# Kernel optimization log

Measured on AMD Instinct MI355X. Metric: run time of the kernel, lower is better.

Reference implementation:

```python
import jax, jax.numpy as jnp
import numpy as np

B = 262144      # batch (many robot-timestep samples)
IN_LEN = 32     # input_len
S = 64          # internal_state_len
M = 32          # message_len
P = 4           # num_ports
H = 100         # hidden_layer_size
L = 50          # lstm_hidden_size
O = 16          # output_len


def _linear_init(key, out_f, in_f):
    # torch.nn.Linear default init: U(-1/sqrt(in_f), 1/sqrt(in_f)) for W and b
    kw, kb = jax.random.split(key)
    bound = 1.0 / np.sqrt(in_f)
    W = jax.random.uniform(kw, (out_f, in_f), jnp.float32, -bound, bound)
    b = jax.random.uniform(kb, (out_f,), jnp.float32, -bound, bound)
    return W, b


def setup_inputs() -> dict:
    key = jax.random.key(0)
    ks = jax.random.split(key, 20)
    obs = jax.random.normal(ks[0], (B, IN_LEN), jnp.float32)
    messages_in = jax.random.normal(ks[1], (P, B, M), jnp.float32)
    h_lstm = jax.random.normal(ks[2], (B, L), jnp.float32)
    c_lstm = jax.random.normal(ks[3], (B, L), jnp.float32)

    W_in, b_in = _linear_init(ks[4], S, IN_LEN)
    # per-port message MLPs, stacked on a leading port axis
    msg1 = [_linear_init(jax.random.fold_in(ks[5], p), H, S) for p in range(P)]
    msg2 = [_linear_init(jax.random.fold_in(ks[6], p), M, H) for p in range(P)]
    msg_W1 = jnp.stack([w for w, _ in msg1])  # [P, H, S]
    msg_b1 = jnp.stack([b for _, b in msg1])  # [P, H]
    msg_W2 = jnp.stack([w for w, _ in msg2])  # [P, M, H]
    msg_b2 = jnp.stack([b for _, b in msg2])  # [P, M]

    # LSTMCell(S + M*P -> L); torch gate order i, f, g, o; init U(-1/sqrt(L), 1/sqrt(L))
    bl = 1.0 / np.sqrt(L)
    W_ih = jax.random.uniform(ks[7], (4 * L, S + M * P), jnp.float32, -bl, bl)
    W_hh = jax.random.uniform(ks[8], (4 * L, L), jnp.float32, -bl, bl)
    b_ih = jax.random.uniform(ks[9], (4 * L,), jnp.float32, -bl, bl)
    b_hh = jax.random.uniform(ks[10], (4 * L,), jnp.float32, -bl, bl)

    W_u1, b_u1 = _linear_init(ks[11], H, L)
    W_u2, b_u2 = _linear_init(ks[12], H, H)
    W_u3, b_u3 = _linear_init(ks[13], S, H)
    W_mu, b_mu = _linear_init(ks[14], O, S)
    W_var, b_var = _linear_init(ks[15], O, S)
    max_logvar = jnp.ones((1, O), jnp.float32) / 2.0
    min_logvar = -jnp.ones((1, O), jnp.float32) * 10.0

    return dict(obs=obs, messages_in=messages_in, h_lstm=h_lstm, c_lstm=c_lstm,
                W_in=W_in, b_in=b_in, msg_W1=msg_W1, msg_b1=msg_b1,
                msg_W2=msg_W2, msg_b2=msg_b2, W_ih=W_ih, W_hh=W_hh,
                b_ih=b_ih, b_hh=b_hh, W_u1=W_u1, b_u1=b_u1, W_u2=W_u2,
                b_u2=b_u2, W_u3=W_u3, b_u3=b_u3, W_mu=W_mu, b_mu=b_mu,
                W_var=W_var, b_var=b_var, max_logvar=max_logvar,
                min_logvar=min_logvar)


def reference(obs, messages_in, h_lstm, c_lstm, W_in, b_in, msg_W1, msg_b1,
              msg_W2, msg_b2, W_ih, W_hh, b_ih, b_hh, W_u1, b_u1, W_u2, b_u2,
              W_u3, b_u3, W_mu, b_mu, W_var, b_var, max_logvar, min_logvar):
    # run_input_function
    x = jax.nn.relu(obs @ W_in.T + b_in)                       # [B, S]

    # compute_messages_out_function: batched over ports (all ports occupied)
    m1 = jax.nn.relu(jnp.einsum('bs,phs->pbh', x, msg_W1) + msg_b1[:, None, :])
    msgs_out = jnp.einsum('pbh,pmh->pbm', m1, msg_W2) + msg_b2[:, None, :]  # [P, B, M]

    # compute_aggregation_function: concat incoming messages along feature dim
    agg = jnp.transpose(messages_in, (1, 0, 2)).reshape(obs.shape[0], -1)  # [B, P*M]
    h_mbar = jnp.concatenate([x, agg], axis=-1)                # [B, S + P*M]

    # status_update_function: one LSTMCell step (torch gate order i, f, g, o)
    gates = h_mbar @ W_ih.T + b_ih + h_lstm @ W_hh.T + b_hh    # [B, 4L]
    i, f, g, o = jnp.split(gates, 4, axis=-1)
    c_new = jax.nn.sigmoid(f) * c_lstm + jax.nn.sigmoid(i) * jnp.tanh(g)
    h_new = jax.nn.sigmoid(o) * jnp.tanh(c_new)                # [B, L]
    h2 = jax.nn.relu(h_new @ W_u1.T + b_u1)
    h2 = jax.nn.relu(h2 @ W_u2.T + b_u2)
    h2 = h2 @ W_u3.T + b_u3                                    # new internal state [B, S]

    # compute_output_function with soft logvar clamping
    mu = h2 @ W_mu.T + b_mu                                    # [B, O]
    logvar = h2 @ W_var.T + b_var
    logvar = max_logvar - jax.nn.softplus(max_logvar - logvar)
    logvar = min_logvar + jax.nn.softplus(logvar - min_logvar)
    var = jnp.exp(logvar)

    msgs_flat = jnp.transpose(msgs_out, (1, 0, 2)).reshape(obs.shape[0], -1)  # [B, P*M]
    # concat all outputs: mu(16) var(16) msgs(128) h2(64) h_new(50) c_new(50) = 324
    return jnp.concatenate([mu, var, msgs_flat, h2, h_new, c_new], axis=-1)
```

## Files before the change

### kernel.cpp

```cpp
#include <hip/hip_runtime.h>

typedef __bf16 bf16_t;
typedef __bf16 bf16x8 __attribute__((ext_vector_type(8)));
typedef float f32x4 __attribute__((ext_vector_type(4)));

#define B_TOTAL 262144
#define OUTC 324
#define ROWS 64

#define OFF_WIN   0
#define OFF_WG    2048
#define OFF_WM1   67584
#define OFF_WM2   96256
#define OFF_WU1   112640
#define OFF_WU2   119808
#define OFF_WU3   134144
#define OFF_WMV2  142336
#define BF16_TOTAL 145920

__global__ void prep_kernel(const float* W_in, const float* msg_W1, const float* msg_W2,
                            const float* W_ih, const float* W_hh, const float* b_ih, const float* b_hh,
                            const float* W_u1, const float* W_u2, const float* W_u3, const float* b_u3f,
                            const float* W_mu, const float* W_var, const float* b_mu, const float* b_var,
                            bf16_t* wb, float* bg, float* bmv) {
  int tid = blockIdx.x * blockDim.x + threadIdx.x;
  int nth = gridDim.x * blockDim.x;
  for (int i = tid; i < 2048; i += nth) wb[OFF_WIN + i] = (bf16_t)W_in[i];
  for (int i = tid; i < 65536; i += nth) {
    int n = i >> 8, k = i & 255;
    int g = n >> 6, j = n & 63;
    float v = 0.f;
    if (j < 50) {
      int r = g * 50 + j;
      if (k < 192) v = W_ih[r * 192 + k];
      else if (k < 242) v = W_hh[r * 50 + (k - 192)];
    }
    wb[OFF_WG + i] = (bf16_t)v;
  }
  for (int i = tid; i < 256; i += nth) {
    int g = i >> 6, j = i & 63;
    bg[i] = (j < 50) ? (b_ih[g * 50 + j] + b_hh[g * 50 + j]) : 0.f;
  }
  for (int i = tid; i < 4 * 112 * 64; i += nth) {
    int p = i / (112 * 64); int rem = i % (112 * 64); int n = rem >> 6, k = rem & 63;
    wb[OFF_WM1 + i] = (bf16_t)((n < 100) ? msg_W1[(p * 100 + n) * 64 + k] : 0.f);
  }
  for (int i = tid; i < 4 * 32 * 128; i += nth) {
    int p = i / (32 * 128); int rem = i % (32 * 128); int n = rem >> 7, k = rem & 127;
    wb[OFF_WM2 + i] = (bf16_t)((k < 100) ? msg_W2[(p * 32 + n) * 100 + k] : 0.f);
  }
  for (int i = tid; i < 112 * 64; i += nth) {
    int n = i >> 6, k = i & 63;
    wb[OFF_WU1 + i] = (bf16_t)((n < 100 && k < 50) ? W_u1[n * 50 + k] : 0.f);
  }
  for (int i = tid; i < 112 * 128; i += nth) {
    int n = i >> 7, k = i & 127;
    wb[OFF_WU2 + i] = (bf16_t)((n < 100 && k < 100) ? W_u2[n * 100 + k] : 0.f);
  }
  for (int i = tid; i < 64 * 128; i += nth) {
    int n = i >> 7, k = i & 127;
    wb[OFF_WU3 + i] = (bf16_t)((k < 100) ? W_u3[n * 100 + k] : 0.f);
  }
  for (int i = tid; i < 32 * 112; i += nth) {
    int o = i / 112, h = i % 112;
    float v = 0.f;
    if (h < 100) {
      const float* wrow = (o < 16) ? (W_mu + o * 64) : (W_var + (o - 16) * 64);
      for (int s = 0; s < 64; s++) v += wrow[s] * W_u3[s * 100 + h];
    }
    wb[OFF_WMV2 + i] = (bf16_t)v;
  }
  for (int i = tid; i < 32; i += nth) {
    int o = i;
    const float* wrow = (o < 16) ? (W_mu + o * 64) : (W_var + (o - 16) * 64);
    float v = (o < 16) ? b_mu[o] : b_var[o - 16];
    for (int s = 0; s < 64; s++) v += wrow[s] * b_u3f[s];
    bmv[o] = v;
  }
}

#define MFMA(a, b, c) __builtin_amdgcn_mfma_f32_16x16x32_bf16((a), (b), (c), 0, 0, 0)

__device__ __forceinline__ float frcp(float x) { return __builtin_amdgcn_rcpf(x); }
__device__ __forceinline__ float fsigmoid(float x) { return frcp(1.f + __expf(-x)); }
__device__ __forceinline__ float ftanh_f(float x) { return 1.f - 2.f * frcp(1.f + __expf(2.f * x)); }
__device__ __forceinline__ float fsoftplus(float x) { return (x > 15.f) ? x : __logf(1.f + __expf(x)); }

__device__ __forceinline__ void barrier_lds() {
  __builtin_amdgcn_sched_barrier(0);
  asm volatile("s_waitcnt lgkmcnt(0)" ::: "memory");
  __builtin_amdgcn_s_barrier();
  __builtin_amdgcn_sched_barrier(0);
}

__device__ __forceinline__ bf16x8 cvt8(const float* __restrict__ p) {
  float4 v0 = *(const float4*)p;
  float4 v1 = *(const float4*)(p + 4);
  bf16x8 r;
  r[0] = (bf16_t)v0.x; r[1] = (bf16_t)v0.y; r[2] = (bf16_t)v0.z; r[3] = (bf16_t)v0.w;
  r[4] = (bf16_t)v1.x; r[5] = (bf16_t)v1.y; r[6] = (bf16_t)v1.z; r[7] = (bf16_t)v1.w;
  return r;
}

__device__ __forceinline__ void stage2(int p, const bf16x8 ax[4][2], bf16_t* dst,
                                       const bf16_t* __restrict__ wb,
                                       const float* __restrict__ msg_b1,
                                       int w, int lr, int kq) {
  for (int nt = w; nt < 7; nt += 4) {
    int nb = nt * 16;
    float bv = (nb + lr < 100) ? msg_b1[p * 100 + nb + lr] : 0.f;
    const bf16_t* Bp = wb + OFF_WM1 + p * 112 * 64 + (nb + lr) * 64 + kq * 8;
    bf16x8 b0 = *(const bf16x8*)Bp;
    bf16x8 b1 = *(const bf16x8*)(Bp + 32);
#pragma unroll
    for (int m = 0; m < 4; m++) {
      f32x4 acc = {bv, bv, bv, bv};
      acc = MFMA(ax[m][0], b0, acc);
      acc = MFMA(ax[m][1], b1, acc);
#pragma unroll
      for (int rr = 0; rr < 4; rr++)
        dst[(m * 16 + kq * 4 + rr) * 120 + nb + lr] = (bf16_t)fmaxf(acc[rr], 0.f);
    }
  }
}

__device__ __forceinline__ void stage3(int p, const bf16_t* src,
                                       const bf16_t* __restrict__ wb,
                                       const float* __restrict__ msg_b2,
                                       float* __restrict__ out,
                                       int row0, int w, int lr, int kq) {
  int nb = (w & 1) * 16;
  float bv = msg_b2[p * 32 + nb + lr];
  const bf16_t* Bp = wb + OFF_WM2 + p * 32 * 128 + (nb + lr) * 128 + kq * 8;
  bf16x8 b[4];
#pragma unroll
  for (int c = 0; c < 4; c++) b[c] = *(const bf16x8*)(Bp + c * 32);
#pragma unroll
  for (int mi = 0; mi < 2; mi++) {
    int m = (w >> 1) + mi * 2;
    f32x4 acc = {bv, bv, bv, bv};
#pragma unroll
    for (int c = 0; c < 4; c++) {
      bf16x8 a;
      if (c < 3) {
        a = *(const bf16x8*)(src + (m * 16 + lr) * 120 + c * 32 + kq * 8);
      } else {
        bf16x8 z = {};
        a = (kq < 2) ? *(const bf16x8*)(src + (m * 16 + lr) * 120 + 96 + kq * 8) : z;
      }
      acc = MFMA(a, b[c], acc);
    }
#pragma unroll
    for (int rr = 0; rr < 4; rr++) {
      size_t row = row0 + m * 16 + kq * 4 + rr;
      out[row * OUTC + 32 + p * 32 + nb + lr] = acc[rr];
    }
  }
}

__global__ __launch_bounds__(256, 2) void fused_kernel(
    const float* __restrict__ obs, const float* __restrict__ msg_in,
    const float* __restrict__ h_lstm, const float* __restrict__ c_lstm,
    const float* __restrict__ b_in, const float* __restrict__ msg_b1,
    const float* __restrict__ msg_b2, const float* __restrict__ b_u1,
    const float* __restrict__ b_u2, const float* __restrict__ b_u3,
    const float* __restrict__ maxlv, const float* __restrict__ minlv,
    const bf16_t* __restrict__ wb, const float* __restrict__ bg,
    const float* __restrict__ bmv, float* __restrict__ out) {
  __shared__ __align__(16) bf16_t xh[ROWS * 72];
  __shared__ __align__(16) bf16_t tA[ROWS * 120];
  __shared__ __align__(16) bf16_t tB[ROWS * 120];

  const int tid = threadIdx.x;
  const int row0 = blockIdx.x * ROWS;
  const int lane = tid & 63;
  const int w = tid >> 6;
  const int lr = lane & 15;
  const int kq = lane >> 4;

  {
    int nb = w * 16;
    float bv = b_in[nb + lr];
    bf16x8 b0 = *(const bf16x8*)(wb + OFF_WIN + (nb + lr) * 32 + kq * 8);
#pragma unroll
    for (int m = 0; m < 4; m++) {
      bf16x8 a0 = cvt8(obs + (size_t)(row0 + m * 16 + lr) * 32 + kq * 8);
      f32x4 acc = {bv, bv, bv, bv};
      acc = MFMA(a0, b0, acc);
#pragma unroll
      for (int rr = 0; rr < 4; rr++)
        xh[(m * 16 + kq * 4 + rr) * 72 + nb + lr] = (bf16_t)fmaxf(acc[rr], 0.f);
    }
  }
  barrier_lds();

  bf16x8 ax[4][2];
#pragma unroll
  for (int m = 0; m < 4; m++)
#pragma unroll
    for (int k = 0; k < 2; k++)
      ax[m][k] = *(const bf16x8*)(xh + (m * 16 + lr) * 72 + k * 32 + kq * 8);

  stage2(0, ax, tA, wb, msg_b1, w, lr, kq);
  barrier_lds();

  stage3(0, tA, wb, msg_b2, out, row0, w, lr, kq);
  stage2(1, ax, tB, wb, msg_b1, w, lr, kq);
  barrier_lds();
  stage3(1, tB, wb, msg_b2, out, row0, w, lr, kq);
  stage2(2, ax, tA, wb, msg_b1, w, lr, kq);
  barrier_lds();
  stage3(2, tA, wb, msg_b2, out, row0, w, lr, kq);
  stage2(3, ax, tB, wb, msg_b1, w, lr, kq);
  barrier_lds();

  {
    const int j = w * 16 + lr;
    float c_pre[4][4];
#pragma unroll
    for (int ms = 0; ms < 4; ms++)
#pragma unroll
      for (int rr = 0; rr < 4; rr++) {
        size_t row = row0 + ms * 16 + kq * 4 + rr;
        c_pre[ms][rr] = (j < 50) ? c_lstm[row * 50 + j] : 0.f;
      }

    stage3(3, tB, wb, msg_b2, out, row0, w, lr, kq);

    f32x4 acc[4][4];
#pragma unroll
    for (int g = 0; g < 4; g++) {
      float bb = bg[g * 64 + j];
      f32x4 bi = {bb, bb, bb, bb};
#pragma unroll
      for (int ms = 0; ms < 4; ms++) acc[g][ms] = bi;
    }
#pragma unroll
    for (int c = 0; c < 8; c++) {
      bf16x8 a[4];
#pragma unroll
      for (int ms = 0; ms < 4; ms++) {
        int lrow = ms * 16 + lr;
        if (c < 2) {
          a[ms] = *(const bf16x8*)(xh + lrow * 72 + c * 32 + kq * 8);
        } else if (c < 6) {
          a[ms] = cvt8(msg_in + ((size_t)(c - 2) * B_TOTAL + row0 + lrow) * 32 + kq * 8);
        } else if (c == 6) {
          a[ms] = cvt8(h_lstm + (size_t)(row0 + lrow) * 50 + kq * 8);
        } else {
          const float* hp = h_lstm + (size_t)(row0 + lrow) * 50;
          if (kq < 2) {
            a[ms] = cvt8(hp + 32 + kq * 8);
          } else if (kq == 2) {
            bf16x8 r = {};
            float2 v = *(const float2*)(hp + 48);
            r[0] = (bf16_t)v.x; r[1] = (bf16_t)v.y;
            a[ms] = r;
          } else {
            bf16x8 r = {};
            a[ms] = r;
          }
        }
      }
      bf16x8 bfr[4];
#pragma unroll
      for (int g = 0; g < 4; g++)
        bfr[g] = *(const bf16x8*)(wb + OFF_WG + (size_t)(g * 64 + j) * 256 + c * 32 + kq * 8);
#pragma unroll
      for (int g = 0; g < 4; g++)
#pragma unroll
        for (int ms = 0; ms < 4; ms++)
          acc[g][ms] = MFMA(a[ms], bfr[g], acc[g][ms]);
    }
#pragma unroll
    for (int ms = 0; ms < 4; ms++) {
#pragma unroll
      for (int rr = 0; rr < 4; rr++) {
        int lrow = ms * 16 + kq * 4 + rr;
        size_t row = row0 + lrow;
        float si = fsigmoid(acc[0][ms][rr]);
        float sf = fsigmoid(acc[1][ms][rr]);
        float gv = ftanh_f(acc[2][ms][rr]);
        float so = fsigmoid(acc[3][ms][rr]);
        float cn = sf * c_pre[ms][rr] + si * gv;
        float hv = so * ftanh_f(cn);
        if (j < 50) {
          out[row * OUTC + 274 + j] = cn;
          out[row * OUTC + 224 + j] = hv;
        }
        tA[lrow * 120 + j] = (bf16_t)((j < 50) ? hv : 0.f);
      }
    }
  }
  barrier_lds();

  for (int nt = w; nt < 7; nt += 4) {
    int nb = nt * 16;
    float bv = (nb + lr < 100) ? b_u1[nb + lr] : 0.f;
    const bf16_t* Bp = wb + OFF_WU1 + (nb + lr) * 64 + kq * 8;
    bf16x8 b0 = *(const bf16x8*)Bp;
    bf16x8 b1 = *(const bf16x8*)(Bp + 32);
#pragma unroll
    for (int m = 0; m < 4; m++) {
      bf16x8 a0 = *(const bf16x8*)(tA + (m * 16 + lr) * 120 + kq * 8);
      bf16x8 a1 = *(const bf16x8*)(tA + (m * 16 + lr) * 120 + kq * 8 + 32);
      f32x4 acc = {bv, bv, bv, bv};
      acc = MFMA(a0, b0, acc);
      acc = MFMA(a1, b1, acc);
#pragma unroll
      for (int rr = 0; rr < 4; rr++)
        tB[(m * 16 + kq * 4 + rr) * 120 + nb + lr] = (bf16_t)fmaxf(acc[rr], 0.f);
    }
  }
  barrier_lds();

  for (int nt = w; nt < 7; nt += 4) {
    int nb = nt * 16;
    float bv = (nb + lr < 100) ? b_u2[nb + lr] : 0.f;
    const bf16_t* Bp = wb + OFF_WU2 + (nb + lr) * 128 + kq * 8;
    bf16x8 b[4];
#pragma unroll
    for (int c = 0; c < 4; c++) b[c] = *(const bf16x8*)(Bp + c * 32);
#pragma unroll
    for (int m = 0; m < 4; m++) {
      f32x4 acc = {bv, bv, bv, bv};
#pragma unroll
      for (int c = 0; c < 4; c++) {
        bf16x8 a;
        if (c < 3) {
          a = *(const bf16x8*)(tB + (m * 16 + lr) * 120 + c * 32 + kq * 8);
        } else {
          bf16x8 z = {};
          a = (kq < 2) ? *(const bf16x8*)(tB + (m * 16 + lr) * 120 + 96 + kq * 8) : z;
        }
        acc = MFMA(a, b[c], acc);
      }
#pragma unroll
      for (int rr = 0; rr < 4; rr++)
        tA[(m * 16 + kq * 4 + rr) * 120 + nb + lr] = (bf16_t)fmaxf(acc[rr], 0.f);
    }
  }
  barrier_lds();

  {
    int nb = w * 16;
    float bv = b_u3[nb + lr];
    const bf16_t* Bp = wb + OFF_WU3 + (nb + lr) * 128 + kq * 8;
    bf16x8 b[4];
#pragma unroll
    for (int c = 0; c < 4; c++) b[c] = *(const bf16x8*)(Bp + c * 32);
#pragma unroll
    for (int m = 0; m < 4; m++) {
      f32x4 acc = {bv, bv, bv, bv};
#pragma unroll
      for (int c = 0; c < 4; c++) {
        bf16x8 a;
        if (c < 3) {
          a = *(const bf16x8*)(tA + (m * 16 + lr) * 120 + c * 32 + kq * 8);
        } else {
          bf16x8 z = {};
          a = (kq < 2) ? *(const bf16x8*)(tA + (m * 16 + lr) * 120 + 96 + kq * 8) : z;
        }
        acc = MFMA(a, b[c], acc);
      }
#pragma unroll
      for (int rr = 0; rr < 4; rr++) {
        size_t row = row0 + m * 16 + kq * 4 + rr;
        out[row * OUTC + 160 + nb + lr] = acc[rr];
      }
    }
  }

  {
    int t = w & 1;
    const bf16_t* Bp = wb + OFF_WMV2 + (t * 16 + lr) * 112 + kq * 8;
    bf16x8 b[4];
#pragma unroll
    for (int c = 0; c < 3; c++) b[c] = *(const bf16x8*)(Bp + c * 32);
    {
      bf16x8 z = {};
      b[3] = (kq < 2) ? *(const bf16x8*)(Bp + 96) : z;
    }
    float bv = bmv[t * 16 + lr];
    float mx = maxlv[lr], mn = minlv[lr];
#pragma unroll
    for (int mi = 0; mi < 2; mi++) {
      int m = (w >> 1) + mi * 2;
      f32x4 acc = {bv, bv, bv, bv};
#pragma unroll
      for (int c = 0; c < 4; c++) {
        bf16x8 a;
        if (c < 3) {
          a = *(const bf16x8*)(tA + (m * 16 + lr) * 120 + c * 32 + kq * 8);
        } else {
          bf16x8 z = {};
          a = (kq < 2) ? *(const bf16x8*)(tA + (m * 16 + lr) * 120 + 96 + kq * 8) : z;
        }
        acc = MFMA(a, b[c], acc);
      }
      if (t == 0) {
#pragma unroll
        for (int rr = 0; rr < 4; rr++) {
          size_t row = row0 + m * 16 + kq * 4 + rr;
          out[row * OUTC + lr] = acc[rr];
        }
      } else {
#pragma unroll
        for (int rr = 0; rr < 4; rr++) {
          size_t row = row0 + m * 16 + kq * 4 + rr;
          float lv = acc[rr];
          lv = mx - fsoftplus(mx - lv);
          lv = mn + fsoftplus(lv - mn);
          out[row * OUTC + 16 + lr] = __expf(lv);
        }
      }
    }
  }
}

extern "C" void kernel_launch(void* const* d_in, const int* in_sizes, int n_in,
                              void* d_out, int out_size, void* d_ws, size_t ws_size,
                              hipStream_t stream) {
  const float* obs   = (const float*)d_in[0];
  const float* msgs  = (const float*)d_in[1];
  const float* h_l   = (const float*)d_in[2];
  const float* c_l   = (const float*)d_in[3];
  const float* W_in  = (const float*)d_in[4];
  const float* b_in  = (const float*)d_in[5];
  const float* mW1   = (const float*)d_in[6];
  const float* mb1   = (const float*)d_in[7];
  const float* mW2   = (const float*)d_in[8];
  const float* mb2   = (const float*)d_in[9];
  const float* W_ih  = (const float*)d_in[10];
  const float* W_hh  = (const float*)d_in[11];
  const float* b_ih  = (const float*)d_in[12];
  const float* b_hh  = (const float*)d_in[13];
  const float* W_u1  = (const float*)d_in[14];
  const float* b_u1  = (const float*)d_in[15];
  const float* W_u2  = (const float*)d_in[16];
  const float* b_u2  = (const float*)d_in[17];
  const float* W_u3  = (const float*)d_in[18];
  const float* b_u3  = (const float*)d_in[19];
  const float* W_mu  = (const float*)d_in[20];
  const float* b_mu  = (const float*)d_in[21];
  const float* W_var = (const float*)d_in[22];
  const float* b_var = (const float*)d_in[23];
  const float* maxlv = (const float*)d_in[24];
  const float* minlv = (const float*)d_in[25];

  bf16_t* wb = (bf16_t*)d_ws;
  float* bg  = (float*)((char*)d_ws + (size_t)BF16_TOTAL * 2);
  float* bmv = bg + 256;

  prep_kernel<<<64, 256, 0, stream>>>(W_in, mW1, mW2, W_ih, W_hh, b_ih, b_hh,
                                      W_u1, W_u2, W_u3, b_u3, W_mu, W_var, b_mu, b_var,
                                      wb, bg, bmv);
  fused_kernel<<<B_TOTAL / ROWS, 256, 0, stream>>>(
      obs, msgs, h_l, c_l, b_in, mb1, mb2, b_u1, b_u2, b_u3,
      maxlv, minlv, wb, bg, bmv, (float*)d_out);
}
```

Measured before the change: 349.0 us.

## Split fused kernel into head and tail kernels passing h_new through output

Splits the single fused kernel into a head kernel (input, message and LSTM stages) and a tail kernel (update MLP and output heads). The tail re-reads h_new from the output buffer in global memory instead of from shared memory, and declares a higher occupancy target in its launch bounds. The aim is to let the lighter tail stage run at higher occupancy, separate from the register-heavy LSTM stage. The cost is an extra kernel launch plus another global round trip of h_new, which is also read back at lower precision.

```diff
diff --git a/kernel.cpp b/kernel.cpp
--- a/kernel.cpp
+++ b/kernel.cpp
@@ -158,15 +158,13 @@
   }
 }
 
-__global__ __launch_bounds__(256, 2) void fused_kernel(
+__global__ __launch_bounds__(256, 2) void head_kernel(
     const float* __restrict__ obs, const float* __restrict__ msg_in,
     const float* __restrict__ h_lstm, const float* __restrict__ c_lstm,
     const float* __restrict__ b_in, const float* __restrict__ msg_b1,
-    const float* __restrict__ msg_b2, const float* __restrict__ b_u1,
-    const float* __restrict__ b_u2, const float* __restrict__ b_u3,
-    const float* __restrict__ maxlv, const float* __restrict__ minlv,
+    const float* __restrict__ msg_b2,
     const bf16_t* __restrict__ wb, const float* __restrict__ bg,
-    const float* __restrict__ bmv, float* __restrict__ out) {
+    float* __restrict__ out) {
   __shared__ __align__(16) bf16_t xh[ROWS * 72];
   __shared__ __align__(16) bf16_t tA[ROWS * 120];
   __shared__ __align__(16) bf16_t tB[ROWS * 120];
@@ -276,8 +274,7 @@
     for (int ms = 0; ms < 4; ms++) {
 #pragma unroll
       for (int rr = 0; rr < 4; rr++) {
-        int lrow = ms * 16 + kq * 4 + rr;
-        size_t row = row0 + lrow;
+        size_t row = row0 + ms * 16 + kq * 4 + rr;
         float si = fsigmoid(acc[0][ms][rr]);
         float sf = fsigmoid(acc[1][ms][rr]);
         float gv = ftanh_f(acc[2][ms][rr]);
@@ -288,11 +285,25 @@
           out[row * OUTC + 274 + j] = cn;
           out[row * OUTC + 224 + j] = hv;
         }
-        tA[lrow * 120 + j] = (bf16_t)((j < 50) ? hv : 0.f);
-      }
-    }
-  }
-  barrier_lds();
+      }
+    }
+  }
+}
+
+__global__ __launch_bounds__(256, 4) void tail_kernel(
+    const float* __restrict__ b_u1, const float* __restrict__ b_u2,
+    const float* __restrict__ b_u3, const float* __restrict__ maxlv,
+    const float* __restrict__ minlv, const bf16_t* __restrict__ wb,
+    const float* __restrict__ bmv, float* __restrict__ out) {
+  __shared__ __align__(16) bf16_t tA[ROWS * 120];
+  __shared__ __align__(16) bf16_t tB[ROWS * 120];
+
+  const int tid = threadIdx.x;
+  const int row0 = blockIdx.x * ROWS;
+  const int lane = tid & 63;
+  const int w = tid >> 6;
+  const int lr = lane & 15;
+  const int kq = lane >> 4;
 
   for (int nt = w; nt < 7; nt += 4) {
     int nb = nt * 16;
@@ -302,14 +313,26 @@
     bf16x8 b1 = *(const bf16x8*)(Bp + 32);
 #pragma unroll
     for (int m = 0; m < 4; m++) {
-      bf16x8 a0 = *(const bf16x8*)(tA + (m * 16 + lr) * 120 + kq * 8);
-      bf16x8 a1 = *(const bf16x8*)(tA + (m * 16 + lr) * 120 + kq * 8 + 32);
+      const float* hp = out + (size_t)(row0 + m * 16 + lr) * OUTC + 224;
+      bf16x8 a0 = cvt8(hp + kq * 8);
+      bf16x8 a1;
+      if (kq < 2) {
+        a1 = cvt8(hp + 32 + kq * 8);
+      } else if (kq == 2) {
+        bf16x8 r = {};
+        float2 v = *(const float2*)(hp + 48);
+        r[0] = (bf16_t)v.x; r[1] = (bf16_t)v.y;
+        a1 = r;
+      } else {
+        bf16x8 r = {};
+        a1 = r;
+      }
       f32x4 acc = {bv, bv, bv, bv};
       acc = MFMA(a0, b0, acc);
       acc = MFMA(a1, b1, acc);
 #pragma unroll
       for (int rr = 0; rr < 4; rr++)
-        tB[(m * 16 + kq * 4 + rr) * 120 + nb + lr] = (bf16_t)fmaxf(acc[rr], 0.f);
+        tA[(m * 16 + kq * 4 + rr) * 120 + nb + lr] = (bf16_t)fmaxf(acc[rr], 0.f);
     }
   }
   barrier_lds();
@@ -318,6 +341,34 @@
     int nb = nt * 16;
     float bv = (nb + lr < 100) ? b_u2[nb + lr] : 0.f;
     const bf16_t* Bp = wb + OFF_WU2 + (nb + lr) * 128 + kq * 8;
+    bf16x8 b[4];
+#pragma unroll
+    for (int c = 0; c < 4; c++) b[c] = *(const bf16x8*)(Bp + c * 32);
+#pragma unroll
+    for (int m = 0; m < 4; m++) {
+      f32x4 acc = {bv, bv, bv, bv};
+#pragma unroll
+      for (int c = 0; c < 4; c++) {
+        bf16x8 a;
+        if (c < 3) {
+          a = *(const bf16x8*)(tA + (m * 16 + lr) * 120 + c * 32 + kq * 8);
+        } else {
+          bf16x8 z = {};
+          a = (kq < 2) ? *(const bf16x8*)(tA + (m * 16 + lr) * 120 + 96 + kq * 8) : z;
+        }
+        acc = MFMA(a, b[c], acc);
+      }
+#pragma unroll
+      for (int rr = 0; rr < 4; rr++)
+        tB[(m * 16 + kq * 4 + rr) * 120 + nb + lr] = (bf16_t)fmaxf(acc[rr], 0.f);
+    }
+  }
+  barrier_lds();
+
+  {
+    int nb = w * 16;
+    float bv = b_u3[nb + lr];
+    const bf16_t* Bp = wb + OFF_WU3 + (nb + lr) * 128 + kq * 8;
     bf16x8 b[4];
 #pragma unroll
     for (int c = 0; c < 4; c++) b[c] = *(const bf16x8*)(Bp + c * 32);
@@ -336,34 +387,6 @@
         acc = MFMA(a, b[c], acc);
       }
 #pragma unroll
-      for (int rr = 0; rr < 4; rr++)
-        tA[(m * 16 + kq * 4 + rr) * 120 + nb + lr] = (bf16_t)fmaxf(acc[rr], 0.f);
-    }
-  }
-  barrier_lds();
-
-  {
-    int nb = w * 16;
-    float bv = b_u3[nb + lr];
-    const bf16_t* Bp = wb + OFF_WU3 + (nb + lr) * 128 + kq * 8;
-    bf16x8 b[4];
-#pragma unroll
-    for (int c = 0; c < 4; c++) b[c] = *(const bf16x8*)(Bp + c * 32);
-#pragma unroll
-    for (int m = 0; m < 4; m++) {
-      f32x4 acc = {bv, bv, bv, bv};
-#pragma unroll
-      for (int c = 0; c < 4; c++) {
-        bf16x8 a;
-        if (c < 3) {
-          a = *(const bf16x8*)(tA + (m * 16 + lr) * 120 + c * 32 + kq * 8);
-        } else {
-          bf16x8 z = {};
-          a = (kq < 2) ? *(const bf16x8*)(tA + (m * 16 + lr) * 120 + 96 + kq * 8) : z;
-        }
-        acc = MFMA(a, b[c], acc);
-      }
-#pragma unroll
       for (int rr = 0; rr < 4; rr++) {
         size_t row = row0 + m * 16 + kq * 4 + rr;
         out[row * OUTC + 160 + nb + lr] = acc[rr];
@@ -391,10 +414,10 @@
       for (int c = 0; c < 4; c++) {
         bf16x8 a;
         if (c < 3) {
-          a = *(const bf16x8*)(tA + (m * 16 + lr) * 120 + c * 32 + kq * 8);
+          a = *(const bf16x8*)(tB + (m * 16 + lr) * 120 + c * 32 + kq * 8);
         } else {
           bf16x8 z = {};
-          a = (kq < 2) ? *(const bf16x8*)(tA + (m * 16 + lr) * 120 + 96 + kq * 8) : z;
+          a = (kq < 2) ? *(const bf16x8*)(tB + (m * 16 + lr) * 120 + 96 + kq * 8) : z;
         }
         acc = MFMA(a, b[c], acc);
       }
@@ -455,7 +478,8 @@
   prep_kernel<<<64, 256, 0, stream>>>(W_in, mW1, mW2, W_ih, W_hh, b_ih, b_hh,
                                       W_u1, W_u2, W_u3, b_u3, W_mu, W_var, b_mu, b_var,
                                       wb, bg, bmv);
-  fused_kernel<<<B_TOTAL / ROWS, 256, 0, stream>>>(
-      obs, msgs, h_l, c_l, b_in, mb1, mb2, b_u1, b_u2, b_u3,
-      maxlv, minlv, wb, bg, bmv, (float*)d_out);
-}
+  head_kernel<<<B_TOTAL / ROWS, 256, 0, stream>>>(
+      obs, msgs, h_l, c_l, b_in, mb1, mb2, wb, bg, (float*)d_out);
+  tail_kernel<<<B_TOTAL / ROWS, 256, 0, stream>>>(
+      b_u1, b_u2, b_u3, maxlv, minlv, wb, bmv, (float*)d_out);
+}
```

Result: slower. 436.1 us (+25.0%).
